# Kernel optimization log

Measured on AMD Instinct MI355X. Metric: run time of the kernel, lower is better.

The kernel has to match this reference:

```python
import jax, jax.numpy as jnp
import numpy as np

DIM = 2048
N_EXPERTS = 8
TOP_K = 2


def setup_inputs() -> dict:
    key = jax.random.key(0)
    ks = jax.random.split(key, 5)
    x = jax.random.normal(ks[0], (4, 4096, DIM), dtype=jnp.float32)
    # Linear(dim, dim, bias=False) stores weight as [out, in]; y = x @ W.T
    W_up = jax.random.normal(ks[1], (DIM, DIM), dtype=jnp.float32) * (1.0 / np.sqrt(DIM))
    W_down = jax.random.normal(ks[2], (DIM, DIM), dtype=jnp.float32) * (1.0 / np.sqrt(DIM))
    W_gate = jax.random.normal(ks[3], (N_EXPERTS, DIM), dtype=jnp.float32) * (1.0 / np.sqrt(DIM))
    # expert_weight: nn.Parameter(torch.randn(dim, dim)), applied as x @ W_expert
    W_expert = jax.random.normal(ks[4], (DIM, DIM), dtype=jnp.float32) * (1.0 / np.sqrt(DIM))
    return {"x": x, "W_up": W_up, "W_down": W_down, "W_gate": W_gate, "W_expert": W_expert}


def reference(x, W_up, W_down, W_gate, W_expert):
    # Gating: logits [B,S,E], top-k routing
    logits = jnp.einsum("bsd,ed->bse", x, W_gate)
    routing_weights, selected_experts = jax.lax.top_k(logits, TOP_K)  # [B,S,K]
    # Shared expert MLP
    shared_out = jnp.einsum("bsd,od->bso", jax.nn.relu(jnp.einsum("bsd,od->bso", x, W_up)), W_down)
    # Mock MoE combine: all selected experts share a single weight matrix, so the
    # dispatch-compute-scatter collapses to a softmax-normalized weighted sum of the
    # same expert output per token (weights sum to 1 over k).
    rw = jax.nn.softmax(routing_weights, axis=-1)  # [B,S,K]
    expert_out = jnp.einsum("bsd,do->bso", x, W_expert)  # shared across selected experts
    moe_out = jnp.sum(rw, axis=-1, keepdims=True) * expert_out
    return shared_out + moe_out
```

## Files before the change

kernel.cpp:

```cpp
#include <hip/hip_runtime.h>
#include <hip/hip_bf16.h>
#include <stdint.h>


#define DIM 2048
#define MTOT 16384

typedef unsigned short u16;
typedef __bf16 bf16x8 __attribute__((ext_vector_type(8)));
typedef float f32x4 __attribute__((ext_vector_type(4)));

__device__ __forceinline__ u16 f2bf(float f) {
    union { float f; unsigned int u; } a; a.f = f;
    unsigned int u = a.u;
    unsigned int r = (u + 0x7fffu + ((u >> 16) & 1u)) >> 16;
    return (u16)r;
}

__device__ __forceinline__ bf16x8 frag_load(const void* p) {
    union { uint4 u; bf16x8 b; } x;
    x.u = *(const uint4*)p;
    return x.b;
}

__global__ void cvt_pack(const float* __restrict__ src, u16* __restrict__ dst,
                         long n4, int dld, int doff) {
    long i = (long)blockIdx.x * blockDim.x + threadIdx.x;
    long stride = (long)gridDim.x * blockDim.x;
    for (; i < n4; i += stride) {
        long e = i << 2;
        long row = e >> 11;
        int col = (int)(e & 2047);
        float4 v = *(const float4*)(src + e);
        union { u16 q[4]; uint2 d; } u;
        u.q[0] = f2bf(v.x); u.q[1] = f2bf(v.y);
        u.q[2] = f2bf(v.z); u.q[3] = f2bf(v.w);
        *(uint2*)(dst + row * (long)dld + doff + col) = u.d;
    }
}

__global__ void cvt_transpose(const float* __restrict__ W, u16* __restrict__ dst) {
    __shared__ float t[32][33];
    int bx = blockIdx.x & 63;
    int by = blockIdx.x >> 6;
    int x = threadIdx.x & 31, y = threadIdx.x >> 5;
    #pragma unroll
    for (int j = 0; j < 32; j += 8)
        t[y + j][x] = W[(size_t)(by * 32 + y + j) * 2048 + bx * 32 + x];
    __syncthreads();
    #pragma unroll
    for (int j = 0; j < 32; j += 8)
        dst[(size_t)(bx * 32 + y + j) * 4096 + 2048 + by * 32 + x] = f2bf(t[x][y + j]);
}

template <int MODE>
__global__ __launch_bounds__(256, 2)
void gemm_bt(const u16* __restrict__ A, const u16* __restrict__ B,
             void* __restrict__ Cptr, int lda, int ldb, int K) {
    __shared__ u16 ldsA[128 * 64];
    __shared__ u16 ldsB[128 * 64];

    const int tid  = threadIdx.x;
    const int lane = tid & 63;
    const int wv   = tid >> 6;
    const int wr   = wv >> 1;
    const int wc   = wv & 1;

    int bid = blockIdx.x;
    int cpx = gridDim.x >> 3;
    int swz = (bid & 7) * cpx + (bid >> 3);
    int tile_n = swz & 15;
    int tile_m = swz >> 4;

    const int rowA0 = tile_m * 128;
    const int rowB0 = tile_n * 128;

    const int r_base = tid >> 3;
    const int c_elt  = (((tid & 7) ^ ((tid >> 3) & 7)) << 3);
    const u16* pA[4];
    const u16* pB[4];
    int stg_off[4];
    #pragma unroll
    for (int s = 0; s < 4; ++s) {
        int r = s * 32 + r_base;
        pA[s] = A + (size_t)(rowA0 + r) * lda + c_elt;
        pB[s] = B + (size_t)(rowB0 + r) * ldb + c_elt;
        stg_off[s] = s * 4096 + (wv << 10);
    }

    f32x4 acc[4][4];
    #pragma unroll
    for (int m = 0; m < 4; ++m)
        #pragma unroll
        for (int n = 0; n < 4; ++n)
            acc[m][n] = (f32x4){0.f, 0.f, 0.f, 0.f};

    const char* cA = (const char*)ldsA;
    const char* cB = (const char*)ldsB;
    const int nK = K >> 6;

    for (int kt = 0; kt < nK; ++kt) {
        const int k0 = kt << 6;
        #pragma unroll
        for (int s = 0; s < 4; ++s) {
            __builtin_amdgcn_global_load_lds(
                (const __attribute__((address_space(1))) void*)(pA[s] + k0),
                (__attribute__((address_space(3))) void*)((char*)ldsA + stg_off[s]),
                16, 0, 0);
            __builtin_amdgcn_global_load_lds(
                (const __attribute__((address_space(1))) void*)(pB[s] + k0),
                (__attribute__((address_space(3))) void*)((char*)ldsB + stg_off[s]),
                16, 0, 0);
        }
        __syncthreads();

        #pragma unroll
        for (int kk = 0; kk < 2; ++kk) {
            const int kb = (kk << 6) + ((lane >> 4) << 4);
            bf16x8 av[4], bv[4];
            #pragma unroll
            for (int i = 0; i < 4; ++i) {
                int ra = (wr << 6) + (i << 4) + (lane & 15);
                av[i] = frag_load(cA + (ra << 7) + (kb ^ ((ra & 7) << 4)));
                int rb = (wc << 6) + (i << 4) + (lane & 15);
                bv[i] = frag_load(cB + (rb << 7) + (kb ^ ((rb & 7) << 4)));
            }
            #pragma unroll
            for (int m = 0; m < 4; ++m)
                #pragma unroll
                for (int n = 0; n < 4; ++n)
                    acc[m][n] = __builtin_amdgcn_mfma_f32_16x16x32_bf16(
                        av[m], bv[n], acc[m][n], 0, 0, 0);
        }
        __syncthreads();
    }

    const int row0 = tile_m * 128 + (wr << 6) + ((lane >> 4) << 2);
    const int col0 = tile_n * 128 + (wc << 6) + (lane & 15);
    if (MODE == 0) {
        u16* C = (u16*)Cptr;
        #pragma unroll
        for (int m = 0; m < 4; ++m)
            #pragma unroll
            for (int r = 0; r < 4; ++r) {
                size_t base = (size_t)(row0 + m * 16 + r) * 4096;
                #pragma unroll
                for (int n = 0; n < 4; ++n)
                    C[base + col0 + n * 16] = f2bf(fmaxf(acc[m][n][r], 0.f));
            }
    } else {
        float* C = (float*)Cptr;
        #pragma unroll
        for (int m = 0; m < 4; ++m)
            #pragma unroll
            for (int r = 0; r < 4; ++r) {
                size_t base = (size_t)(row0 + m * 16 + r) * 2048;
                #pragma unroll
                for (int n = 0; n < 4; ++n)
                    C[base + col0 + n * 16] = acc[m][n][r];
            }
    }
}

extern "C" void kernel_launch(void* const* d_in, const int* in_sizes, int n_in,
                              void* d_out, int out_size, void* d_ws, size_t ws_size,
                              hipStream_t stream) {
    const float* x        = (const float*)d_in[0];
    const float* W_up     = (const float*)d_in[1];
    const float* W_down   = (const float*)d_in[2];
    const float* W_expert = (const float*)d_in[4];

    u16* Abig = (u16*)d_ws;
    u16* Bbig = Abig + (size_t)MTOT * 4096;
    u16* Wup  = Bbig + (size_t)DIM * 4096;

    cvt_pack<<<2048, 256, 0, stream>>>(x, Abig, (long)MTOT * DIM / 4, 4096, 2048);
    cvt_pack<<<1024, 256, 0, stream>>>(W_up, Wup, (long)DIM * DIM / 4, 2048, 0);
    cvt_pack<<<1024, 256, 0, stream>>>(W_down, Bbig, (long)DIM * DIM / 4, 4096, 0);
    cvt_transpose<<<4096, 256, 0, stream>>>(W_expert, Bbig);

    gemm_bt<0><<<2048, 256, 0, stream>>>(Abig + 2048, Wup, Abig, 4096, 2048, 2048);
    gemm_bt<1><<<2048, 256, 0, stream>>>(Abig, Bbig, d_out, 4096, 4096, 4096);
}
```

Baseline: 436.4 us.

## Use 256x256 tiles with double-buffered LDS and quadrant-interleaved MFMA pipeline

Replaces the 128x128 single-buffered GEMM with a 256x256-tile kernel using 512 threads, a double-buffered 128KB LDS and explicit vmcnt/lgkmcnt waits. Global-to-LDS loads for the next K-step are interleaved with MFMA work on four output quadrants of the current step, and s_setprio raises priority around the MFMA sections. The aim is to hide global load latency and increase arithmetic intensity per byte loaded. The cost is heavy LDS use that likely limits occupancy to one block per CU, plus fragile hand-counted waitcnt values.

```diff
diff --git a/kernel.cpp b/kernel.cpp
--- a/kernel.cpp
+++ b/kernel.cpp
@@ -54,112 +54,187 @@
 }
 
 template <int MODE>
-__global__ __launch_bounds__(256, 2)
-void gemm_bt(const u16* __restrict__ A, const u16* __restrict__ B,
+__global__ __launch_bounds__(512, 2)
+void gemm256(const u16* __restrict__ A, const u16* __restrict__ B,
              void* __restrict__ Cptr, int lda, int ldb, int K) {
-    __shared__ u16 ldsA[128 * 64];
-    __shared__ u16 ldsB[128 * 64];
+    __shared__ char lds[2][65536];
 
     const int tid  = threadIdx.x;
     const int lane = tid & 63;
     const int wv   = tid >> 6;
-    const int wr   = wv >> 1;
-    const int wc   = wv & 1;
+    const int wr   = wv >> 2;
+    const int wc   = wv & 3;
 
     int bid = blockIdx.x;
     int cpx = gridDim.x >> 3;
     int swz = (bid & 7) * cpx + (bid >> 3);
-    int tile_n = swz & 15;
-    int tile_m = swz >> 4;
-
-    const int rowA0 = tile_m * 128;
-    const int rowB0 = tile_n * 128;
-
-    const int r_base = tid >> 3;
-    const int c_elt  = (((tid & 7) ^ ((tid >> 3) & 7)) << 3);
-    const u16* pA[4];
-    const u16* pB[4];
-    int stg_off[4];
-    #pragma unroll
-    for (int s = 0; s < 4; ++s) {
-        int r = s * 32 + r_base;
-        pA[s] = A + (size_t)(rowA0 + r) * lda + c_elt;
-        pB[s] = B + (size_t)(rowB0 + r) * ldb + c_elt;
-        stg_off[s] = s * 4096 + (wv << 10);
-    }
-
-    f32x4 acc[4][4];
-    #pragma unroll
-    for (int m = 0; m < 4; ++m)
+    int tile_n = swz & 7;
+    int tile_m = swz >> 3;
+
+    const int rowA0 = tile_m * 256;
+    const int rowB0 = tile_n * 256;
+
+    const int r_sub = tid >> 3;
+    const int c_src = ((tid & 7) ^ (r_sub & 7)) << 3;
+    const u16* pAb = A + (size_t)(rowA0 + r_sub) * lda + c_src;
+    const u16* pBb = B + (size_t)(rowB0 + r_sub) * ldb + c_src;
+
+    f32x4 acc[2][2][4][2];
+    #pragma unroll
+    for (int a = 0; a < 2; ++a)
         #pragma unroll
-        for (int n = 0; n < 4; ++n)
-            acc[m][n] = (f32x4){0.f, 0.f, 0.f, 0.f};
-
-    const char* cA = (const char*)ldsA;
-    const char* cB = (const char*)ldsB;
-    const int nK = K >> 6;
-
-    for (int kt = 0; kt < nK; ++kt) {
-        const int k0 = kt << 6;
-        #pragma unroll
-        for (int s = 0; s < 4; ++s) {
-            __builtin_amdgcn_global_load_lds(
-                (const __attribute__((address_space(1))) void*)(pA[s] + k0),
-                (__attribute__((address_space(3))) void*)((char*)ldsA + stg_off[s]),
-                16, 0, 0);
-            __builtin_amdgcn_global_load_lds(
-                (const __attribute__((address_space(1))) void*)(pB[s] + k0),
-                (__attribute__((address_space(3))) void*)((char*)ldsB + stg_off[s]),
-                16, 0, 0);
-        }
-        __syncthreads();
-
-        #pragma unroll
-        for (int kk = 0; kk < 2; ++kk) {
-            const int kb = (kk << 6) + ((lane >> 4) << 4);
-            bf16x8 av[4], bv[4];
-            #pragma unroll
-            for (int i = 0; i < 4; ++i) {
-                int ra = (wr << 6) + (i << 4) + (lane & 15);
-                av[i] = frag_load(cA + (ra << 7) + (kb ^ ((ra & 7) << 4)));
-                int rb = (wc << 6) + (i << 4) + (lane & 15);
-                bv[i] = frag_load(cB + (rb << 7) + (kb ^ ((rb & 7) << 4)));
-            }
+        for (int b = 0; b < 2; ++b)
             #pragma unroll
             for (int m = 0; m < 4; ++m)
                 #pragma unroll
-                for (int n = 0; n < 4; ++n)
-                    acc[m][n] = __builtin_amdgcn_mfma_f32_16x16x32_bf16(
-                        av[m], bv[n], acc[m][n], 0, 0, 0);
-        }
-        __syncthreads();
+                for (int n = 0; n < 2; ++n)
+                    acc[a][b][m][n] = (f32x4){0.f, 0.f, 0.f, 0.f};
+
+    bf16x8 av[4][2];
+    bf16x8 bv[2][2];
+    const int kA = (lane >> 4) << 4;
+
+#define STAGE_A(H, KOFF, BUF) do {                                              \
+    const u16* _s = pAb + (size_t)((H) * 128) * lda + (KOFF);                   \
+    __builtin_amdgcn_global_load_lds(                                           \
+        (const __attribute__((address_space(1))) void*)_s,                      \
+        (__attribute__((address_space(3))) void*)((char*)lds[BUF] + (H)*16384 + (wv<<10)), \
+        16, 0, 0);                                                              \
+    __builtin_amdgcn_global_load_lds(                                           \
+        (const __attribute__((address_space(1))) void*)(_s + (size_t)64 * lda), \
+        (__attribute__((address_space(3))) void*)((char*)lds[BUF] + (H)*16384 + 8192 + (wv<<10)), \
+        16, 0, 0);                                                              \
+  } while (0)
+
+#define STAGE_B(H, KOFF, BUF) do {                                              \
+    const u16* _s = pBb + (size_t)((H) * 128) * ldb + (KOFF);                   \
+    __builtin_amdgcn_global_load_lds(                                           \
+        (const __attribute__((address_space(1))) void*)_s,                      \
+        (__attribute__((address_space(3))) void*)((char*)lds[BUF] + 32768 + (H)*16384 + (wv<<10)), \
+        16, 0, 0);                                                              \
+    __builtin_amdgcn_global_load_lds(                                           \
+        (const __attribute__((address_space(1))) void*)(_s + (size_t)64 * ldb), \
+        (__attribute__((address_space(3))) void*)((char*)lds[BUF] + 32768 + (H)*16384 + 8192 + (wv<<10)), \
+        16, 0, 0);                                                              \
+  } while (0)
+
+#define DSREAD_A(MH, CUR) do {                                                  \
+    _Pragma("unroll")                                                           \
+    for (int m = 0; m < 4; ++m) {                                               \
+        int ra = (wr << 6) + (m << 4) + (lane & 15);                            \
+        const char* _b = (const char*)lds[CUR] + (MH)*16384 + (ra << 7);        \
+        int sw = (ra & 7) << 4;                                                 \
+        av[m][0] = frag_load(_b + (kA ^ sw));                                   \
+        av[m][1] = frag_load(_b + ((64 + kA) ^ sw));                            \
+    } } while (0)
+
+#define DSREAD_B(NH, CUR) do {                                                  \
+    _Pragma("unroll")                                                           \
+    for (int n = 0; n < 2; ++n) {                                               \
+        int rb = (wc << 5) + (n << 4) + (lane & 15);                            \
+        const char* _b = (const char*)lds[CUR] + 32768 + (NH)*16384 + (rb << 7);\
+        int sw = (rb & 7) << 4;                                                 \
+        bv[n][0] = frag_load(_b + (kA ^ sw));                                   \
+        bv[n][1] = frag_load(_b + ((64 + kA) ^ sw));                            \
+    } } while (0)
+
+#define MFMA_Q(MH, NH) do {                                                     \
+    __builtin_amdgcn_s_setprio(1);                                              \
+    _Pragma("unroll")                                                           \
+    for (int m = 0; m < 4; ++m)                                                 \
+        _Pragma("unroll")                                                       \
+        for (int n = 0; n < 2; ++n) {                                           \
+            acc[MH][NH][m][n] = __builtin_amdgcn_mfma_f32_16x16x32_bf16(        \
+                av[m][0], bv[n][0], acc[MH][NH][m][n], 0, 0, 0);                \
+            acc[MH][NH][m][n] = __builtin_amdgcn_mfma_f32_16x16x32_bf16(        \
+                av[m][1], bv[n][1], acc[MH][NH][m][n], 0, 0, 0);                \
+        }                                                                       \
+    __builtin_amdgcn_s_setprio(0);                                              \
+  } while (0)
+
+#define WAIT_VM(N) asm volatile("s_waitcnt vmcnt(" #N ")" ::: "memory")
+#define WAIT_LGKM() do {                                                        \
+    asm volatile("s_waitcnt lgkmcnt(0)" ::: "memory");                          \
+    __builtin_amdgcn_sched_barrier(0);                                          \
+  } while (0)
+#define BAR() __builtin_amdgcn_s_barrier()
+
+    STAGE_A(0, 0, 0);
+    STAGE_B(0, 0, 0);
+    STAGE_B(1, 0, 0);
+    STAGE_A(1, 0, 0);
+    WAIT_VM(4);
+    BAR();
+
+    const int nK = K >> 6;
+    int cur = 0;
+    for (int t = 0; t < nK - 1; ++t) {
+        const int koff = (t + 1) << 6;
+        const int nxt = cur ^ 1;
+        DSREAD_A(0, cur); DSREAD_B(0, cur);
+        STAGE_A(0, koff, nxt);
+        WAIT_VM(4); BAR(); WAIT_LGKM();
+        MFMA_Q(0, 0);
+        BAR();
+        DSREAD_B(1, cur);
+        STAGE_B(0, koff, nxt);
+        WAIT_VM(4); BAR(); WAIT_LGKM();
+        MFMA_Q(0, 1);
+        BAR();
+        DSREAD_A(1, cur);
+        STAGE_B(1, koff, nxt);
+        WAIT_VM(6); BAR(); WAIT_LGKM();
+        MFMA_Q(1, 1);
+        BAR();
+        DSREAD_B(0, cur);
+        STAGE_A(1, koff, nxt);
+        WAIT_VM(4); BAR(); WAIT_LGKM();
+        MFMA_Q(1, 0);
+        BAR();
+        cur = nxt;
     }
 
-    const int row0 = tile_m * 128 + (wr << 6) + ((lane >> 4) << 2);
-    const int col0 = tile_n * 128 + (wc << 6) + (lane & 15);
-    if (MODE == 0) {
-        u16* C = (u16*)Cptr;
+    DSREAD_A(0, cur); DSREAD_B(0, cur);
+    WAIT_VM(2); BAR(); WAIT_LGKM();
+    MFMA_Q(0, 0);
+    DSREAD_B(1, cur);
+    WAIT_VM(0); BAR(); WAIT_LGKM();
+    MFMA_Q(0, 1);
+    DSREAD_A(1, cur);
+    WAIT_LGKM();
+    MFMA_Q(1, 1);
+    DSREAD_B(0, cur);
+    WAIT_LGKM();
+    MFMA_Q(1, 0);
+
+    #pragma unroll
+    for (int mh = 0; mh < 2; ++mh)
         #pragma unroll
         for (int m = 0; m < 4; ++m)
             #pragma unroll
             for (int r = 0; r < 4; ++r) {
-                size_t base = (size_t)(row0 + m * 16 + r) * 4096;
+                int row = rowA0 + mh * 128 + (wr << 6) + (m << 4) + ((lane >> 4) << 2) + r;
                 #pragma unroll
-                for (int n = 0; n < 4; ++n)
-                    C[base + col0 + n * 16] = f2bf(fmaxf(acc[m][n][r], 0.f));
+                for (int nh = 0; nh < 2; ++nh)
+                    #pragma unroll
+                    for (int n = 0; n < 2; ++n) {
+                        int col = tile_n * 256 + nh * 128 + (wc << 5) + (n << 4) + (lane & 15);
+                        float v = acc[mh][nh][m][n][r];
+                        if (MODE == 0) {
+                            ((u16*)Cptr)[(size_t)row * 4096 + col] = f2bf(fmaxf(v, 0.f));
+                        } else {
+                            ((float*)Cptr)[(size_t)row * 2048 + col] = v;
+                        }
+                    }
             }
-    } else {
-        float* C = (float*)Cptr;
-        #pragma unroll
-        for (int m = 0; m < 4; ++m)
-            #pragma unroll
-            for (int r = 0; r < 4; ++r) {
-                size_t base = (size_t)(row0 + m * 16 + r) * 2048;
-                #pragma unroll
-                for (int n = 0; n < 4; ++n)
-                    C[base + col0 + n * 16] = acc[m][n][r];
-            }
-    }
+#undef STAGE_A
+#undef STAGE_B
+#undef DSREAD_A
+#undef DSREAD_B
+#undef MFMA_Q
+#undef WAIT_VM
+#undef WAIT_LGKM
+#undef BAR
 }
 
 extern "C" void kernel_launch(void* const* d_in, const int* in_sizes, int n_in,
@@ -179,6 +254,6 @@
     cvt_pack<<<1024, 256, 0, stream>>>(W_down, Bbig, (long)DIM * DIM / 4, 4096, 0);
     cvt_transpose<<<4096, 256, 0, stream>>>(W_expert, Bbig);
 
-    gemm_bt<0><<<2048, 256, 0, stream>>>(Abig + 2048, Wup, Abig, 4096, 2048, 2048);
-    gemm_bt<1><<<2048, 256, 0, stream>>>(Abig, Bbig, d_out, 4096, 4096, 4096);
-}
+    gemm256<0><<<512, 512, 0, stream>>>(Abig + 2048, Wup, Abig, 4096, 2048, 2048);
+    gemm256<1><<<512, 512, 0, stream>>>(Abig, Bbig, d_out, 4096, 4096, 4096);
+}
```

After: 411.8 us. 1.06x faster.
